# Kernel tuning notes

Hardware: AMD Instinct MI355X
Metric: run time of the kernel (lower is better)

Reference implementation:

```python
import jax, jax.numpy as jnp
import numpy as np

LRELU_SLOPE = 0.1  # correlate_operator uses F.leaky_relu_(corr, 0.1)


def _conv2d(x, w, b):
    # x: [B,Ci,H,W], w: [Co,Ci,kh,kw], stride 1, padding SAME (=padding=1 for 3x3)
    y = jax.lax.conv_general_dilated(x, w, (1, 1), 'SAME',
                                     dimension_numbers=('NCHW', 'OIHW', 'NCHW'))
    return y + b[None, :, None, None]


def correlate(x1, x2):
    # spatial_correlation_sample(x1, x2, kernel_size=3, patch_size=1, stride=1,
    # padding=1): with patch_size=1 the only displacement is (0,0), so the cost
    # volume is a 3x3 window sum of the per-pixel channel dot product.
    # Then divided by C and leaky_relu(0.1) as in correlate_operator.
    prod = jnp.sum(x1 * x2, axis=1, keepdims=True)  # [B,1,H,W]
    box = jnp.ones((1, 1, 3, 3), prod.dtype)
    corr = jax.lax.conv_general_dilated(prod, box, (1, 1), 'SAME',
                                        dimension_numbers=('NCHW', 'OIHW', 'NCHW'))
    corr = corr / x1.shape[1]
    return jnp.where(corr > 0, corr, LRELU_SLOPE * corr)


def deform_conv2d(x, offset, w):
    # mmcv DeformConv2d: kernel 3x3, stride 1, pad 1, dilation 1, deform_groups=1,
    # bias=False. offset: [B, 2*kh*kw, H, W], per kernel tap k: (dy_k, dx_k).
    B, Cin, H, W = x.shape
    O, _, kh, kw = w.shape
    K = kh * kw
    off = offset.reshape(B, K, 2, H, W)
    dy, dx = off[:, :, 0], off[:, :, 1]  # [B,K,H,W]
    ky, kx = jnp.meshgrid(jnp.arange(kh), jnp.arange(kw), indexing='ij')
    # sampling position: p + p_k + offset_k (pad=1 cancels the kernel-center shift)
    y = jnp.arange(H, dtype=x.dtype)[None, None, :, None] \
        + (ky.reshape(-1) - kh // 2).astype(x.dtype)[None, :, None, None] + dy
    xx = jnp.arange(W, dtype=x.dtype)[None, None, None, :] \
        + (kx.reshape(-1) - kw // 2).astype(x.dtype)[None, :, None, None] + dx
    y0 = jnp.floor(y)
    x0 = jnp.floor(xx)
    wy = (y - y0)[:, None]   # [B,1,K,H,W]
    wx = (xx - x0)[:, None]
    y0i = y0.astype(jnp.int32)
    x0i = x0.astype(jnp.int32)
    xf = x.reshape(B, Cin, H * W)

    def gather(yi, xi):
        valid = (yi >= 0) & (yi < H) & (xi >= 0) & (xi < W)  # zero padding outside
        idx = jnp.clip(yi, 0, H - 1) * W + jnp.clip(xi, 0, W - 1)
        v = jnp.take_along_axis(xf, idx.reshape(B, 1, K * H * W), axis=2)
        return v.reshape(B, Cin, K, H, W) * valid.astype(x.dtype)[:, None]

    v00 = gather(y0i, x0i)
    v01 = gather(y0i, x0i + 1)
    v10 = gather(y0i + 1, x0i)
    v11 = gather(y0i + 1, x0i + 1)
    samp = (v00 * (1 - wy) * (1 - wx) + v01 * (1 - wy) * wx
            + v10 * wy * (1 - wx) + v11 * wy * wx)  # [B,Cin,K,H,W]
    return jnp.einsum('bckhw,ock->bohw', samp, w.reshape(O, Cin, K))


def setup_inputs() -> dict:
    key = jax.random.key(0)
    ks = jax.random.split(key, 10)
    B, C, H, W = 4, 256, 64, 64
    s = 0.02
    return {
        'x_ref': jax.random.normal(ks[0], (B, C, H, W), jnp.float32),
        'x_next': jax.random.normal(ks[1], (B, C, H, W), jnp.float32),
        'w1': jax.random.normal(ks[2], (256, 1, 3, 3), jnp.float32) * s,
        'b1': jax.random.normal(ks[3], (256,), jnp.float32) * s,
        'w2': jax.random.normal(ks[4], (256, 256, 3, 3), jnp.float32) * s,
        'b2': jax.random.normal(ks[5], (256,), jnp.float32) * s,
        'w3': jax.random.normal(ks[6], (18, 256, 3, 3), jnp.float32) * s,
        'b3': jax.random.normal(ks[7], (18,), jnp.float32) * s,
        'w_dcn': jax.random.normal(ks[8], (256, 256, 3, 3), jnp.float32) * s,
        'idx': 4,
    }


def reference(x_ref, x_next, w1, b1, w2, b2, w3, b3, w_dcn, idx):
    # idx=4 -> corr_patch_size=1 (consistent with conv1 in_channels)
    corr = correlate(x_next, x_ref)                      # [B,1,H,W]
    h = jax.nn.relu(_conv2d(corr, w1, b1))               # [B,256,H,W]
    h = jax.nn.relu(_conv2d(h, w2, b2))                  # [B,256,H,W]
    offset = jax.nn.relu(_conv2d(h, w3, b3))             # [B,18,H,W]
    x_ref_cal = jax.nn.relu(deform_conv2d(x_ref, offset, w_dcn))
    return 0.5 * (x_next + x_ref_cal)
```

## Files before the change

### kernel.cpp

```cpp
#include <hip/hip_runtime.h>

typedef __attribute__((ext_vector_type(8))) short short8v;
typedef __attribute__((ext_vector_type(4))) float f32x4;
typedef __attribute__((ext_vector_type(2))) float f32x2;
typedef __attribute__((ext_vector_type(4))) unsigned int u32x4;

constexpr int Bsz = 4;
constexpr int Hh = 64, Wwd = 64;
constexpr int HWp = Hh * Wwd;
constexpr int NPIX = Bsz * HWp;
constexpr int HH = 66;
constexpr int HPIX = HH * HH;
constexpr int Kdim = 2304;
constexpr int NSTEP = 36;

constexpr size_t B_H1H  = 0;
constexpr size_t HALO_BYTES = (size_t)Bsz * HPIX * 256 * 2;
constexpr size_t B_H2H  = B_H1H + HALO_BYTES;
constexpr size_t B_XTH  = B_H2H + HALO_BYTES;
constexpr size_t B_PROD = B_XTH + HALO_BYTES;
constexpr size_t B_OFFP = B_PROD + (size_t)NPIX * 4;
constexpr size_t B_WB2  = B_OFFP + (size_t)NPIX * 32 * 4;
constexpr size_t B_WBD  = B_WB2 + (size_t)256 * Kdim * 2;
constexpr size_t B_WB3  = B_WBD + (size_t)256 * Kdim * 2;

static __device__ __forceinline__ unsigned short f2bf(float f) {
    unsigned u = __builtin_bit_cast(unsigned, f);
    u += 0x7FFFu + ((u >> 16) & 1u);
    return (unsigned short)(u >> 16);
}
static __device__ __forceinline__ unsigned cvt_pk_bf16(float lo, float hi) {
    unsigned r;
    asm("v_cvt_pk_bf16_f32 %0, %1, %2" : "=v"(r) : "v"(lo), "v"(hi));
    return r;
}
static __device__ __forceinline__ f32x2 pk_mul(f32x2 a, f32x2 b) {
    f32x2 d;
    asm("v_pk_mul_f32 %0, %1, %2" : "=v"(d) : "v"(a), "v"(b));
    return d;
}
static __device__ __forceinline__ f32x2 pk_fma(f32x2 a, f32x2 b, f32x2 c) {
    f32x2 d;
    asm("v_pk_fma_f32 %0, %1, %2, %3" : "=v"(d) : "v"(a), "v"(b), "v"(c));
    return d;
}
static __device__ __forceinline__ f32x2 unpack2(unsigned u) {
    f32x2 v;
    v.x = __builtin_bit_cast(float, u << 16);
    v.y = __builtin_bit_cast(float, u & 0xFFFF0000u);
    return v;
}
static __device__ __forceinline__ void gload_lds16(const void* g, void* l) {
    __builtin_amdgcn_global_load_lds((const __attribute__((address_space(1))) unsigned int*)g,
                                     (__attribute__((address_space(3))) unsigned int*)l, 16, 0, 0);
}
static __device__ __forceinline__ int swz(int u) {
    return (((u & 7) ^ ((u >> 3) & 7)) << 3);
}

__global__ void k_zero_ring(unsigned short* h1h, unsigned short* h2h, unsigned short* xth,
                            float* prod) {
    int blk = blockIdx.x;
    if (blk >= 3120) {
        unsigned* p = (unsigned*)prod + (size_t)(blk - 3120) * 128 + threadIdx.x;
        *p = 0;
        return;
    }
    int img = blk / 260;
    int rp = blk - img * 260;
    int buf = img >> 2, b = img & 3;
    int y, x;
    if (rp < 66) { y = 0; x = rp; }
    else if (rp < 132) { y = 65; x = rp - 66; }
    else { int s2 = rp - 132; y = 1 + (s2 >> 1); x = (s2 & 1) * 65; }
    unsigned short* base = (buf == 0) ? h1h : (buf == 1) ? h2h : xth;
    unsigned* p = (unsigned*)(base + ((size_t)b * HPIX + y * HH + x) * 256);
    p[threadIdx.x] = 0;
}

__global__ void k_prodx(const float* __restrict__ xr, const float* __restrict__ xn,
                        unsigned short* __restrict__ xth, float* __restrict__ prod) {
    __shared__ float t[32][33];
    __shared__ float red[8][33];
    int b = blockIdx.z;
    int c0 = blockIdx.y * 32;
    int y = blockIdx.x >> 1, x0 = (blockIdx.x & 1) * 32;
    int tx = threadIdx.x, ty = threadIdx.y;
    float part = 0.f;
#pragma unroll
    for (int i = 0; i < 32; i += 8) {
        size_t idx = ((size_t)b * 256 + c0 + ty + i) * HWp + y * Wwd + x0 + tx;
        float vr = xr[idx];
        float vn = xn[idx];
        t[ty + i][tx] = vr;
        part = fmaf(vr, vn, part);
    }
    red[ty][tx] = part;
    __syncthreads();
#pragma unroll
    for (int i = 0; i < 32; i += 8)
        xth[((size_t)b * HPIX + (y + 1) * HH + (x0 + ty + i + 1)) * 256 + c0 + tx] =
            f2bf(t[tx][ty + i]);
    if (ty == 0) {
        float s = red[0][tx] + red[1][tx] + red[2][tx] + red[3][tx] +
                  red[4][tx] + red[5][tx] + red[6][tx] + red[7][tx];
        atomicAdd(&prod[b * HWp + y * Wwd + x0 + tx], s);
    }
}

__global__ __launch_bounds__(256) void k_conv1c(const float* __restrict__ prod,
                                                const float* __restrict__ w1,
                                                const float* __restrict__ b1,
                                                unsigned short* __restrict__ h1h) {
    __shared__ float pp[5][36];
    __shared__ float pt[3][34];
    int px0 = blockIdx.x * 32;
    int b = px0 >> 12, y = (px0 & 4095) >> 6, x0 = px0 & 63;
    int tid = threadIdx.x;
    if (tid < 180) {
        int i = tid / 36, j = tid - i * 36;
        int yy = y - 2 + i, xx = x0 - 2 + j;
        float v = 0.f;
        if (yy >= 0 && yy < Hh && xx >= 0 && xx < Wwd) v = prod[b * HWp + yy * Wwd + xx];
        pp[i][j] = v;
    }
    __syncthreads();
    if (tid < 102) {
        int i = tid / 34, j = tid - i * 34;
        int yy = y - 1 + i, xx = x0 - 1 + j;
        float v = 0.f;
        if (yy >= 0 && yy < Hh && xx >= 0 && xx < Wwd) {
            float s = pp[i][j]     + pp[i][j + 1]     + pp[i][j + 2] +
                      pp[i + 1][j] + pp[i + 1][j + 1] + pp[i + 1][j + 2] +
                      pp[i + 2][j] + pp[i + 2][j + 1] + pp[i + 2][j + 2];
            s *= (1.0f / 256.0f);
            v = (s > 0.f) ? s : 0.1f * s;
        }
        pt[i][j] = v;
    }
    float wl[9];
#pragma unroll
    for (int k = 0; k < 9; ++k) wl[k] = w1[tid * 9 + k];
    float bias = b1[tid];
    __syncthreads();
    for (int p = 0; p < 32; ++p) {
        float acc = bias;
#pragma unroll
        for (int ky = 0; ky < 3; ++ky)
#pragma unroll
            for (int kx = 0; kx < 3; ++kx) acc = fmaf(pt[ky][p + kx], wl[ky * 3 + kx], acc);
        acc = fmaxf(acc, 0.f);
        h1h[((size_t)b * HPIX + (y + 1) * HH + (x0 + p + 1)) * 256 + tid] = f2bf(acc);
    }
}

__global__ void k_packall(const float* __restrict__ w2, const float* __restrict__ wd,
                          const float* __restrict__ w3,
                          unsigned short* __restrict__ wb2f, unsigned short* __restrict__ wbdf,
                          unsigned short* __restrict__ wb3) {
    int blk = blockIdx.x;
    if (blk < 4608) {
        const float* w = (blk < 2304) ? w2 : wd;
        unsigned short* out = (blk < 2304) ? wb2f : wbdf;
        int i = (blk % 2304) * 256 + threadIdx.x;
        int e = i & 7;
        int lane = (i >> 3) & 63;
        int mi = (i >> 9) & 1;
        int kf = (i >> 10) & 1;
        int rest = i >> 11;
        int s = rest % 36;
        int wv = rest / 36;
        int o = wv * 32 + mi * 16 + (lane & 15);
        int kk = s * 64 + (kf * 4 + (lane >> 4)) * 8 + e;
        int c = kk & 255, tap = kk >> 8;
        out[i] = f2bf(w[((size_t)o * 256 + c) * 9 + tap]);
    } else {
        int i = (blk - 4608) * 256 + threadIdx.x;
        int o = i / Kdim;
        int r = i - o * Kdim;
        int k = r >> 8, c = r & 255;
        float v = (o < 18) ? w3[((size_t)o * 256 + c) * 9 + k] : 0.f;
        wb3[i] = f2bf(v);
    }
}

__global__ __launch_bounds__(512) void k_conv2g(const unsigned short* __restrict__ h1h,
                                                const unsigned short* __restrict__ wbf,
                                                const float* __restrict__ bias,
                                                unsigned short* __restrict__ h2h) {
    __shared__ short S_s[2][64 * 64];
    const int tid = threadIdx.x;
    const int bid = blockIdx.x;
    const int px0 = ((bid & 7) * 32 + (bid >> 3)) * 64;
    const int b = px0 >> 12;
    const unsigned short* hb = h1h + (size_t)b * HPIX * 256;
    const int pxl = tid >> 3;
    const int px = px0 + pxl;
    const int y = (px & 4095) >> 6, x = px & 63;
    const int u0 = tid & 7;
    const int lane = tid & 63, wv = tid >> 6;
    const unsigned short* wfb = wbf + (size_t)wv * NSTEP * 2048 + lane * 8;
    const unsigned short* abase0 = hb + (size_t)((y + 1) * HH + (x + 1)) * 256 + u0 * 8;

    f32x4 acc[4][2] = {};
    u32x4 wA[4], wB[4], aA, aB;
    float bia[2];
#pragma unroll
    for (int oi = 0; oi < 2; ++oi) bia[oi] = bias[wv * 32 + oi * 16 + (lane & 15)];

    const int wr0 = pxl * 64 + ((u0 ^ (pxl & 7)) << 3);

    auto WLOAD = [&](int s, u32x4 (&wreg)[4]) {
#pragma unroll
        for (int f = 0; f < 4; ++f)
            wreg[f] = *(const u32x4*)(wfb + ((size_t)s * 4 + f) * 512);
    };
    auto ALOAD = [&](int s) {
        int tap = s >> 2, chunk = s & 3;
        int aoff = ((tap / 3 - 1) * HH + (tap % 3 - 1)) * 256 + chunk * 64;
        return *(const u32x4*)(abase0 + aoff);
    };

    {
        u32x4 a0 = ALOAD(0);
        WLOAD(0, wA);
        *(u32x4*)&S_s[0][wr0] = a0;
        aA = ALOAD(1);
        asm volatile("s_waitcnt lgkmcnt(0)" ::: "memory");
    }

    auto ITER = [&](int s, u32x4 (&wcur)[4], u32x4 (&wnxt)[4], u32x4& aCur, u32x4& aNxt,
                    short* SBc, short* SBn) {
        __builtin_amdgcn_s_barrier();
        __builtin_amdgcn_sched_barrier(0);
        if (s + 1 < NSTEP) *(u32x4*)&SBn[wr0] = aCur;
        if (s + 2 < NSTEP) aNxt = ALOAD(s + 2);
        if (s + 1 < NSTEP) WLOAD(s + 1, wnxt);
        short8v af[4][2];
#pragma unroll
        for (int pi = 0; pi < 4; ++pi) {
            int row = pi * 16 + (lane & 15);
#pragma unroll
            for (int kf = 0; kf < 2; ++kf) {
                int c8 = kf * 4 + (lane >> 4);
                af[pi][kf] = *(const short8v*)&SBc[row * 64 + ((c8 ^ (row & 7)) << 3)];
            }
        }
        __builtin_amdgcn_s_setprio(1);
#pragma unroll
        for (int kf = 0; kf < 2; ++kf)
#pragma unroll
            for (int pi = 0; pi < 4; ++pi)
#pragma unroll
                for (int oi = 0; oi < 2; ++oi)
                    acc[pi][oi] = __builtin_amdgcn_mfma_f32_16x16x32_bf16(
                        af[pi][kf], __builtin_bit_cast(short8v, wcur[kf * 2 + oi]),
                        acc[pi][oi], 0, 0, 0);
        __builtin_amdgcn_s_setprio(0);
        asm volatile("s_waitcnt lgkmcnt(0)" ::: "memory");
    };

    for (int s2 = 0; s2 < NSTEP; s2 += 2) {
        ITER(s2, wA, wB, aA, aB, &S_s[0][0], &S_s[1][0]);
        ITER(s2 + 1, wB, wA, aB, aA, &S_s[1][0], &S_s[0][0]);
    }

#pragma unroll
    for (int pi = 0; pi < 4; ++pi) {
#pragma unroll
        for (int j = 0; j < 4; ++j) {
            int p2 = px0 + pi * 16 + (lane >> 4) * 4 + j;
            int yy = (p2 & 4095) >> 6, xx = p2 & 63;
            unsigned short* dst = h2h + ((size_t)b * HPIX + (yy + 1) * HH + (xx + 1)) * 256;
#pragma unroll
            for (int oi = 0; oi < 2; ++oi) {
                int o = wv * 32 + oi * 16 + (lane & 15);
                dst[o] = f2bf(fmaxf(acc[pi][oi][j] + bia[oi], 0.f));
            }
        }
    }
}

__global__ __launch_bounds__(256) void k_conv3g(const unsigned short* __restrict__ h2h,
                                                const unsigned short* __restrict__ wb,
                                                const float* __restrict__ bias,
                                                float* __restrict__ offp) {
    __shared__ short A_s[2][64 * 64];
    __shared__ short B_s[2][32 * 64];
    const int tid = threadIdx.x;
    const int px0 = blockIdx.x * 64;
    const int b = px0 >> 12;
    const unsigned short* hb = h2h + (size_t)b * HPIX * 256;

    const unsigned short* abase[2];
#pragma unroll
    for (int i = 0; i < 2; ++i) {
        int u = i * 256 + tid;
        int pxl = u >> 3;
        int pxg = px0 + pxl;
        int y = (pxg & 4095) >> 6, x = pxg & 63;
        abase[i] = hb + (size_t)((y + 1) * HH + (x + 1)) * 256 + swz(u);
    }
    const unsigned short* bbase = wb + (size_t)(tid >> 3) * Kdim + swz(tid);

    const int lane = tid & 63, wv = tid >> 6;
    f32x4 acc[2] = {};

    auto STAGE = [&](int s, int buf) {
        int tap = s >> 2, chunk = s & 3;
        int delta = ((tap / 3 - 1) * HH + (tap % 3 - 1)) * 256 + chunk * 64;
        short* Ab = &A_s[buf][0];
#pragma unroll
        for (int i = 0; i < 2; ++i) gload_lds16(abase[i] + delta, Ab + (i * 256 + tid) * 8);
        gload_lds16(bbase + s * 64, &B_s[buf][tid * 8]);
    };

    STAGE(0, 0);
    __syncthreads();
    for (int s = 0; s < NSTEP; ++s) {
        int cur = s & 1;
        if (s + 1 < NSTEP) STAGE(s + 1, cur ^ 1);
        const short* Ab = &A_s[cur][0];
        const short* Bb = &B_s[cur][0];
        short8v af[2], bf[2][2];
#pragma unroll
        for (int kf = 0; kf < 2; ++kf) {
            int row = wv * 16 + (lane & 15);
            int c8 = kf * 4 + (lane >> 4);
            af[kf] = *(const short8v*)&Ab[row * 64 + ((c8 ^ (row & 7)) << 3)];
        }
#pragma unroll
        for (int ni = 0; ni < 2; ++ni) {
            int row = ni * 16 + (lane & 15);
#pragma unroll
            for (int kf = 0; kf < 2; ++kf) {
                int c8 = kf * 4 + (lane >> 4);
                bf[ni][kf] = *(const short8v*)&Bb[row * 64 + ((c8 ^ (row & 7)) << 3)];
            }
        }
#pragma unroll
        for (int kf = 0; kf < 2; ++kf)
#pragma unroll
            for (int ni = 0; ni < 2; ++ni)
                acc[ni] = __builtin_amdgcn_mfma_f32_16x16x32_bf16(af[kf], bf[ni][kf], acc[ni], 0, 0, 0);
        __syncthreads();
    }
#pragma unroll
    for (int j = 0; j < 4; ++j) {
        int px = px0 + wv * 16 + (lane >> 4) * 4 + j;
#pragma unroll
        for (int ni = 0; ni < 2; ++ni) {
            int o = ni * 16 + (lane & 15);
            float bv = (o < 18) ? bias[o] : 0.f;
            offp[(size_t)px * 32 + o] = fmaxf(acc[ni][j] + bv, 0.f);
        }
    }
}

__global__ __launch_bounds__(512) void k_dcng(const unsigned short* __restrict__ xth,
                                              const float* __restrict__ offp,
                                              const unsigned short* __restrict__ wbf,
                                              const float* __restrict__ xn,
                                              float* __restrict__ out) {
    __shared__ short S_s[2][64 * 64];
    const int tid = threadIdx.x;
    const int bid = blockIdx.x;
    const int px0 = ((bid & 7) * 32 + (bid >> 3)) * 64;
    const int b = px0 >> 12;
    const unsigned short* xb = xth + (size_t)b * HPIX * 256;
    const int pxl = tid >> 3;
    const int px = px0 + pxl;
    const int y = (px & 4095) >> 6, x = px & 63;
    const int u0 = tid & 7;
    const int lane = tid & 63, wv = tid >> 6;
    const unsigned short* wfb = wbf + (size_t)wv * NSTEP * 2048 + lane * 8;
    const float2* offv = (const float2*)offp;

    f32x4 acc[2][4] = {};
    u32x4 wA[4], wB[4];
    u32x4 gA[4], gB[4];
    const int wr0 = pxl * 64 + ((u0 ^ (pxl & 7)) << 3);

    const unsigned short* pcorner[4];
    f32x2 wpair[4];
    float2 offn;

    auto SETUP = [&](int tap, float dyo, float dxo) {
        int ky = tap / 3 - 1, kx = tap % 3 - 1;
        float ypos = (float)(y + ky) + dyo;
        float xpos = (float)(x + kx) + dxo;
        float y0f = floorf(ypos), x0f = floorf(xpos);
        float wy = ypos - y0f, wx = xpos - x0f;
        int y0 = (int)y0f, x0 = (int)x0f;
        bool y0v = (y0 >= 0) && (y0 < Hh), y1v = (y0 + 1 >= 0) && (y0 + 1 < Hh);
        bool x0v = (x0 >= 0) && (x0 < Wwd), x1v = (x0 + 1 >= 0) && (x0 + 1 < Wwd);
        int hy0 = min(max(y0, -1), 64) + 1, hy1 = min(max(y0 + 1, -1), 64) + 1;
        int hx0 = min(max(x0, -1), 64) + 1, hx1 = min(max(x0 + 1, -1), 64) + 1;
        float w0 = (1.f - wy) * (1.f - wx) * (float)(y0v && x0v);
        float w1 = (1.f - wy) * wx * (float)(y0v && x1v);
        float w2 = wy * (1.f - wx) * (float)(y1v && x0v);
        float w3 = wy * wx * (float)(y1v && x1v);
        wpair[0] = (f32x2){w0, w0};
        wpair[1] = (f32x2){w1, w1};
        wpair[2] = (f32x2){w2, w2};
        wpair[3] = (f32x2){w3, w3};
        pcorner[0] = xb + (size_t)((hy0 * HH + hx0) * 256) + u0 * 8;
        pcorner[1] = xb + (size_t)((hy0 * HH + hx1) * 256) + u0 * 8;
        pcorner[2] = xb + (size_t)((hy1 * HH + hx0) * 256) + u0 * 8;
        pcorner[3] = xb + (size_t)((hy1 * HH + hx1) * 256) + u0 * 8;
    };
    auto WLOAD = [&](int s, u32x4 (&wreg)[4]) {
#pragma unroll
        for (int f = 0; f < 4; ++f)
            wreg[f] = *(const u32x4*)(wfb + ((size_t)s * 4 + f) * 512);
    };
    auto GISSUE = [&](int s, u32x4 (&g)[4]) {
        const int nco = (s & 3) * 64;
#pragma unroll
        for (int c = 0; c < 4; ++c) g[c] = *(const u32x4*)(pcorner[c] + nco);
    };
    auto COMBINE_WRITE = [&](u32x4 (&g)[4], short* SBn) {
        u32x4 res;
#pragma unroll
        for (int qd = 0; qd < 4; ++qd) {
            f32x2 a = pk_mul(unpack2(g[0][qd]), wpair[0]);
            a = pk_fma(unpack2(g[1][qd]), wpair[1], a);
            a = pk_fma(unpack2(g[2][qd]), wpair[2], a);
            a = pk_fma(unpack2(g[3][qd]), wpair[3], a);
            res[qd] = cvt_pk_bf16(a.x, a.y);
        }
        *(u32x4*)&SBn[wr0] = res;
    };

    {
        float2 o0 = offv[(size_t)px * 16];
        SETUP(0, o0.x, o0.y);
        u32x4 g0[4];
        GISSUE(0, g0);
        WLOAD(0, wA);
        COMBINE_WRITE(g0, &S_s[0][0]);
        GISSUE(1, gA);
        asm volatile("s_waitcnt lgkmcnt(0)" ::: "memory");
    }

    auto ITER = [&](int s, u32x4 (&wcur)[4], u32x4 (&wnxt)[4],
                    u32x4 (&gcur)[4], u32x4 (&gnxt)[4], short* SBc, short* SBn) {
        __builtin_amdgcn_s_barrier();
        __builtin_amdgcn_sched_barrier(0);
        if (s + 1 < NSTEP) COMBINE_WRITE(gcur, SBn);
        if ((s & 3) == 0 && (s >> 2) + 1 < 9)
            offn = offv[(size_t)px * 16 + (s >> 2) + 1];
        if ((s & 3) == 2 && s + 2 < NSTEP)
            SETUP((s + 2) >> 2, offn.x, offn.y);
        if (s + 2 < NSTEP) GISSUE(s + 2, gnxt);
        if (s + 1 < NSTEP) WLOAD(s + 1, wnxt);
        short8v sf[4][2];
#pragma unroll
        for (int ni = 0; ni < 4; ++ni) {
            int row = ni * 16 + (lane & 15);
#pragma unroll
            for (int kf = 0; kf < 2; ++kf) {
                int c8 = kf * 4 + (lane >> 4);
                sf[ni][kf] = *(const short8v*)&SBc[row * 64 + ((c8 ^ (row & 7)) << 3)];
            }
        }
        __builtin_amdgcn_s_setprio(1);
#pragma unroll
        for (int kf = 0; kf < 2; ++kf)
#pragma unroll
            for (int mi = 0; mi < 2; ++mi)
#pragma unroll
                for (int ni = 0; ni < 4; ++ni)
                    acc[mi][ni] = __builtin_amdgcn_mfma_f32_16x16x32_bf16(
                        __builtin_bit_cast(short8v, wcur[kf * 2 + mi]), sf[ni][kf],
                        acc[mi][ni], 0, 0, 0);
        __builtin_amdgcn_s_setprio(0);
        asm volatile("s_waitcnt lgkmcnt(0)" ::: "memory");
    };

    for (int s2 = 0; s2 < NSTEP; s2 += 2) {
        ITER(s2, wA, wB, gA, gB, &S_s[0][0], &S_s[1][0]);
        ITER(s2 + 1, wB, wA, gB, gA, &S_s[1][0], &S_s[0][0]);
    }

#pragma unroll
    for (int mi = 0; mi < 2; ++mi) {
        int o = wv * 32 + mi * 16 + (lane >> 4) * 4;
#pragma unroll
        for (int j = 0; j < 4; ++j) {
            size_t rowbase = ((size_t)b * 256 + o + j) * HWp;
#pragma unroll
            for (int ni = 0; ni < 4; ++ni) {
                int p2 = (px0 + ni * 16 + (lane & 15)) & 4095;
                size_t idx = rowbase + p2;
                out[idx] = 0.5f * (xn[idx] + fmaxf(acc[mi][ni][j], 0.f));
            }
        }
    }
}

extern "C" void kernel_launch(void* const* d_in, const int* in_sizes, int n_in,
                              void* d_out, int out_size, void* d_ws, size_t ws_size,
                              hipStream_t stream) {
    const float* x_ref  = (const float*)d_in[0];
    const float* x_next = (const float*)d_in[1];
    const float* w1 = (const float*)d_in[2];
    const float* b1 = (const float*)d_in[3];
    const float* w2 = (const float*)d_in[4];
    const float* b2 = (const float*)d_in[5];
    const float* w3 = (const float*)d_in[6];
    const float* b3 = (const float*)d_in[7];
    const float* wd = (const float*)d_in[8];
    float* out = (float*)d_out;
    char* ws = (char*)d_ws;

    unsigned short* h1h = (unsigned short*)(ws + B_H1H);
    unsigned short* h2h = (unsigned short*)(ws + B_H2H);
    unsigned short* xth = (unsigned short*)(ws + B_XTH);
    float* prod = (float*)(ws + B_PROD);
    float* offp = (float*)(ws + B_OFFP);
    unsigned short* wb2f = (unsigned short*)(ws + B_WB2);
    unsigned short* wbdf = (unsigned short*)(ws + B_WBD);
    unsigned short* wb3  = (unsigned short*)(ws + B_WB3);

    k_zero_ring<<<3120 + 128, 128, 0, stream>>>(h1h, h2h, xth, prod);
    k_prodx<<<dim3(128, 8, Bsz), dim3(32, 8), 0, stream>>>(x_ref, x_next, xth, prod);
    k_packall<<<4896, 256, 0, stream>>>(w2, wd, w3, wb2f, wbdf, wb3);
    k_conv1c<<<NPIX / 32, 256, 0, stream>>>(prod, w1, b1, h1h);
    k_conv2g<<<256, 512, 0, stream>>>(h1h, wb2f, b2, h2h);
    k_conv3g<<<256, 256, 0, stream>>>(h2h, wb3, b3, offp);
    k_dcng<<<256, 512, 0, stream>>>(xth, offp, wbdf, x_next, out);
}
```

Before: 111.8 us.

## Split conv2 output channels across two blocks and double K-step per barrier in DCN

conv2 now launches 512 blocks of 256 threads, each handling 64 pixels by 128 output channels, so every thread stages two 16-byte activation chunks. This gives more blocks for the 256 CUs at the cost of loading the activation tile twice. The deformable conv now handles two K-steps per barrier with a four-buffer LDS ring and doubled weight and gather registers. That halves the barrier count and deepens prefetch, but raises register and LDS pressure, which may lower occupancy.

```diff
diff --git a/kernel.cpp b/kernel.cpp
--- a/kernel.cpp
+++ b/kernel.cpp
@@ -184,57 +184,68 @@
     }
 }
 
-__global__ __launch_bounds__(512) void k_conv2g(const unsigned short* __restrict__ h1h,
+__global__ __launch_bounds__(256) void k_conv2g(const unsigned short* __restrict__ h1h,
                                                 const unsigned short* __restrict__ wbf,
                                                 const float* __restrict__ bias,
                                                 unsigned short* __restrict__ h2h) {
     __shared__ short S_s[2][64 * 64];
     const int tid = threadIdx.x;
     const int bid = blockIdx.x;
-    const int px0 = ((bid & 7) * 32 + (bid >> 3)) * 64;
+    const int lin = (bid & 7) * 64 + (bid >> 3);
+    const int px0 = (lin >> 1) * 64;
+    const int oblk = lin & 1;
     const int b = px0 >> 12;
     const unsigned short* hb = h1h + (size_t)b * HPIX * 256;
-    const int pxl = tid >> 3;
+    const int pxl = tid >> 2;
     const int px = px0 + pxl;
     const int y = (px & 4095) >> 6, x = px & 63;
-    const int u0 = tid & 7;
+    const int u0 = (tid & 3) * 2;
     const int lane = tid & 63, wv = tid >> 6;
-    const unsigned short* wfb = wbf + (size_t)wv * NSTEP * 2048 + lane * 8;
+    const int ot = oblk * 4 + wv;
+    const unsigned short* wfb = wbf + (size_t)ot * NSTEP * 2048 + lane * 8;
     const unsigned short* abase0 = hb + (size_t)((y + 1) * HH + (x + 1)) * 256 + u0 * 8;
 
     f32x4 acc[4][2] = {};
-    u32x4 wA[4], wB[4], aA, aB;
+    u32x4 wA[4], wB[4], aA0, aA1, aB0, aB1;
     float bia[2];
 #pragma unroll
-    for (int oi = 0; oi < 2; ++oi) bia[oi] = bias[wv * 32 + oi * 16 + (lane & 15)];
+    for (int oi = 0; oi < 2; ++oi) bia[oi] = bias[ot * 32 + oi * 16 + (lane & 15)];
 
     const int wr0 = pxl * 64 + ((u0 ^ (pxl & 7)) << 3);
+    const int wr1 = pxl * 64 + (((u0 + 1) ^ (pxl & 7)) << 3);
 
     auto WLOAD = [&](int s, u32x4 (&wreg)[4]) {
 #pragma unroll
         for (int f = 0; f < 4; ++f)
             wreg[f] = *(const u32x4*)(wfb + ((size_t)s * 4 + f) * 512);
     };
-    auto ALOAD = [&](int s) {
+    auto ALOAD = [&](int s, u32x4& a0, u32x4& a1) {
         int tap = s >> 2, chunk = s & 3;
         int aoff = ((tap / 3 - 1) * HH + (tap % 3 - 1)) * 256 + chunk * 64;
-        return *(const u32x4*)(abase0 + aoff);
+        a0 = *(const u32x4*)(abase0 + aoff);
+        a1 = *(const u32x4*)(abase0 + aoff + 8);
     };
 
     {
-        u32x4 a0 = ALOAD(0);
+        u32x4 a0, a1;
+        ALOAD(0, a0, a1);
         WLOAD(0, wA);
         *(u32x4*)&S_s[0][wr0] = a0;
-        aA = ALOAD(1);
+        *(u32x4*)&S_s[0][wr1] = a1;
+        ALOAD(1, aA0, aA1);
         asm volatile("s_waitcnt lgkmcnt(0)" ::: "memory");
     }
 
-    auto ITER = [&](int s, u32x4 (&wcur)[4], u32x4 (&wnxt)[4], u32x4& aCur, u32x4& aNxt,
+    auto ITER = [&](int s, u32x4 (&wcur)[4], u32x4 (&wnxt)[4],
+                    u32x4& aC0, u32x4& aC1, u32x4& aN0, u32x4& aN1,
                     short* SBc, short* SBn) {
         __builtin_amdgcn_s_barrier();
         __builtin_amdgcn_sched_barrier(0);
-        if (s + 1 < NSTEP) *(u32x4*)&SBn[wr0] = aCur;
-        if (s + 2 < NSTEP) aNxt = ALOAD(s + 2);
+        if (s + 1 < NSTEP) {
+            *(u32x4*)&SBn[wr0] = aC0;
+            *(u32x4*)&SBn[wr1] = aC1;
+        }
+        if (s + 2 < NSTEP) ALOAD(s + 2, aN0, aN1);
         if (s + 1 < NSTEP) WLOAD(s + 1, wnxt);
         short8v af[4][2];
 #pragma unroll
@@ -261,8 +272,8 @@
     };
 
     for (int s2 = 0; s2 < NSTEP; s2 += 2) {
-        ITER(s2, wA, wB, aA, aB, &S_s[0][0], &S_s[1][0]);
-        ITER(s2 + 1, wB, wA, aB, aA, &S_s[1][0], &S_s[0][0]);
+        ITER(s2, wA, wB, aA0, aA1, aB0, aB1, &S_s[0][0], &S_s[1][0]);
+        ITER(s2 + 1, wB, wA, aB0, aB1, aA0, aA1, &S_s[1][0], &S_s[0][0]);
     }
 
 #pragma unroll
@@ -274,7 +285,7 @@
             unsigned short* dst = h2h + ((size_t)b * HPIX + (yy + 1) * HH + (xx + 1)) * 256;
 #pragma unroll
             for (int oi = 0; oi < 2; ++oi) {
-                int o = wv * 32 + oi * 16 + (lane & 15);
+                int o = ot * 32 + oi * 16 + (lane & 15);
                 dst[o] = f2bf(fmaxf(acc[pi][oi][j] + bia[oi], 0.f));
             }
         }
@@ -362,7 +373,7 @@
                                               const unsigned short* __restrict__ wbf,
                                               const float* __restrict__ xn,
                                               float* __restrict__ out) {
-    __shared__ short S_s[2][64 * 64];
+    __shared__ short S_s[4][64 * 64];
     const int tid = threadIdx.x;
     const int bid = blockIdx.x;
     const int px0 = ((bid & 7) * 32 + (bid >> 3)) * 64;
@@ -377,8 +388,8 @@
     const float2* offv = (const float2*)offp;
 
     f32x4 acc[2][4] = {};
-    u32x4 wA[4], wB[4];
-    u32x4 gA[4], gB[4];
+    u32x4 wA[2][4], wB[2][4];
+    u32x4 g[2][4];
     const int wr0 = pxl * 64 + ((u0 ^ (pxl & 7)) << 3);
 
     const unsigned short* pcorner[4];
@@ -414,19 +425,19 @@
         for (int f = 0; f < 4; ++f)
             wreg[f] = *(const u32x4*)(wfb + ((size_t)s * 4 + f) * 512);
     };
-    auto GISSUE = [&](int s, u32x4 (&g)[4]) {
+    auto GISSUE = [&](int s, u32x4 (&gr)[4]) {
         const int nco = (s & 3) * 64;
 #pragma unroll
-        for (int c = 0; c < 4; ++c) g[c] = *(const u32x4*)(pcorner[c] + nco);
-    };
-    auto COMBINE_WRITE = [&](u32x4 (&g)[4], short* SBn) {
+        for (int c = 0; c < 4; ++c) gr[c] = *(const u32x4*)(pcorner[c] + nco);
+    };
+    auto COMBINE_WRITE = [&](u32x4 (&gr)[4], short* SBn) {
         u32x4 res;
 #pragma unroll
         for (int qd = 0; qd < 4; ++qd) {
-            f32x2 a = pk_mul(unpack2(g[0][qd]), wpair[0]);
-            a = pk_fma(unpack2(g[1][qd]), wpair[1], a);
-            a = pk_fma(unpack2(g[2][qd]), wpair[2], a);
-            a = pk_fma(unpack2(g[3][qd]), wpair[3], a);
+            f32x2 a = pk_mul(unpack2(gr[0][qd]), wpair[0]);
+            a = pk_fma(unpack2(gr[1][qd]), wpair[1], a);
+            a = pk_fma(unpack2(gr[2][qd]), wpair[2], a);
+            a = pk_fma(unpack2(gr[3][qd]), wpair[3], a);
             res[qd] = cvt_pk_bf16(a.x, a.y);
         }
         *(u32x4*)&SBn[wr0] = res;
@@ -435,52 +446,69 @@
     {
         float2 o0 = offv[(size_t)px * 16];
         SETUP(0, o0.x, o0.y);
-        u32x4 g0[4];
+        u32x4 g0[4], g1[4];
         GISSUE(0, g0);
-        WLOAD(0, wA);
+        GISSUE(1, g1);
+        WLOAD(0, wA[0]);
+        WLOAD(1, wA[1]);
         COMBINE_WRITE(g0, &S_s[0][0]);
-        GISSUE(1, gA);
+        COMBINE_WRITE(g1, &S_s[1][0]);
+        GISSUE(2, g[0]);
+        GISSUE(3, g[1]);
+        offn = offv[(size_t)px * 16 + 1];
         asm volatile("s_waitcnt lgkmcnt(0)" ::: "memory");
     }
 
-    auto ITER = [&](int s, u32x4 (&wcur)[4], u32x4 (&wnxt)[4],
-                    u32x4 (&gcur)[4], u32x4 (&gnxt)[4], short* SBc, short* SBn) {
+    auto ITER2 = [&](int s, u32x4 (&wcur)[2][4], u32x4 (&wnxt)[2][4], short* SBc, short* SBn) {
         __builtin_amdgcn_s_barrier();
         __builtin_amdgcn_sched_barrier(0);
-        if (s + 1 < NSTEP) COMBINE_WRITE(gcur, SBn);
-        if ((s & 3) == 0 && (s >> 2) + 1 < 9)
-            offn = offv[(size_t)px * 16 + (s >> 2) + 1];
-        if ((s & 3) == 2 && s + 2 < NSTEP)
-            SETUP((s + 2) >> 2, offn.x, offn.y);
-        if (s + 2 < NSTEP) GISSUE(s + 2, gnxt);
-        if (s + 1 < NSTEP) WLOAD(s + 1, wnxt);
-        short8v sf[4][2];
-#pragma unroll
-        for (int ni = 0; ni < 4; ++ni) {
-            int row = ni * 16 + (lane & 15);
-#pragma unroll
-            for (int kf = 0; kf < 2; ++kf) {
-                int c8 = kf * 4 + (lane >> 4);
-                sf[ni][kf] = *(const short8v*)&SBc[row * 64 + ((c8 ^ (row & 7)) << 3)];
+        if (s + 2 < NSTEP) {
+            COMBINE_WRITE(g[0], SBn);
+            COMBINE_WRITE(g[1], SBn + 64 * 64);
+        }
+        if ((s & 3) == 0 && s + 4 < NSTEP)
+            SETUP((s + 4) >> 2, offn.x, offn.y);
+        if ((s & 3) == 2 && ((s + 8) >> 2) < 9)
+            offn = offv[(size_t)px * 16 + ((s + 8) >> 2)];
+        if (s + 4 < NSTEP) {
+            GISSUE(s + 4, g[0]);
+            GISSUE(s + 5, g[1]);
+        }
+        if (s + 2 < NSTEP) {
+            WLOAD(s + 2, wnxt[0]);
+            WLOAD(s + 3, wnxt[1]);
+        }
+#pragma unroll
+        for (int half = 0; half < 2; ++half) {
+            const short* SB = SBc + half * 64 * 64;
+            short8v sf[4][2];
+#pragma unroll
+            for (int ni = 0; ni < 4; ++ni) {
+                int row = ni * 16 + (lane & 15);
+#pragma unroll
+                for (int kf = 0; kf < 2; ++kf) {
+                    int c8 = kf * 4 + (lane >> 4);
+                    sf[ni][kf] = *(const short8v*)&SB[row * 64 + ((c8 ^ (row & 7)) << 3)];
+                }
             }
-        }
-        __builtin_amdgcn_s_setprio(1);
-#pragma unroll
-        for (int kf = 0; kf < 2; ++kf)
-#pragma unroll
-            for (int mi = 0; mi < 2; ++mi)
-#pragma unroll
-                for (int ni = 0; ni < 4; ++ni)
-                    acc[mi][ni] = __builtin_amdgcn_mfma_f32_16x16x32_bf16(
-                        __builtin_bit_cast(short8v, wcur[kf * 2 + mi]), sf[ni][kf],
-                        acc[mi][ni], 0, 0, 0);
-        __builtin_amdgcn_s_setprio(0);
+            __builtin_amdgcn_s_setprio(1);
+#pragma unroll
+            for (int kf = 0; kf < 2; ++kf)
+#pragma unroll
+                for (int mi = 0; mi < 2; ++mi)
+#pragma unroll
+                    for (int ni = 0; ni < 4; ++ni)
+                        acc[mi][ni] = __builtin_amdgcn_mfma_f32_16x16x32_bf16(
+                            __builtin_bit_cast(short8v, wcur[half][kf * 2 + mi]), sf[ni][kf],
+                            acc[mi][ni], 0, 0, 0);
+            __builtin_amdgcn_s_setprio(0);
+        }
         asm volatile("s_waitcnt lgkmcnt(0)" ::: "memory");
     };
 
-    for (int s2 = 0; s2 < NSTEP; s2 += 2) {
-        ITER(s2, wA, wB, gA, gB, &S_s[0][0], &S_s[1][0]);
-        ITER(s2 + 1, wB, wA, gB, gA, &S_s[1][0], &S_s[0][0]);
+    for (int s4 = 0; s4 < NSTEP; s4 += 4) {
+        ITER2(s4, wA, wB, &S_s[0][0], &S_s[2][0]);
+        ITER2(s4 + 2, wB, wA, &S_s[2][0], &S_s[0][0]);
     }
 
 #pragma unroll
@@ -527,7 +555,7 @@
     k_prodx<<<dim3(128, 8, Bsz), dim3(32, 8), 0, stream>>>(x_ref, x_next, xth, prod);
     k_packall<<<4896, 256, 0, stream>>>(w2, wd, w3, wb2f, wbdf, wb3);
     k_conv1c<<<NPIX / 32, 256, 0, stream>>>(prod, w1, b1, h1h);
-    k_conv2g<<<256, 512, 0, stream>>>(h1h, wb2f, b2, h2h);
+    k_conv2g<<<512, 256, 0, stream>>>(h1h, wb2f, b2, h2h);
     k_conv3g<<<256, 256, 0, stream>>>(h2h, wb3, b3, offp);
     k_dcng<<<256, 512, 0, stream>>>(xth, offp, wbdf, x_next, out);
 }
```

Result: faster. 108.9 us (-2.6%).
